# Kernel tuning notes

Measured on AMD Instinct MI355X. Metric: run time of the kernel, lower is better.

Reference implementation:

```python
import jax, jax.numpy as jnp
import numpy as np


def setup_inputs() -> dict:
    key = jax.random.key(0)
    k1, k2 = jax.random.split(key)
    B, T, F, H = 64, 512, 512, 1024
    x = jax.random.normal(k1, (B, T, F), dtype=jnp.float32)
    W = jax.random.normal(k2, (F + H, H), dtype=jnp.float32) * (1.0 / np.sqrt(F + H))
    b = jnp.zeros((H,), dtype=jnp.float32)
    return {"x": x, "W": W, "b": b}


def reference(x, W, b):
    # Vanilla tanh RNN: state_t = tanh([x_t, state_{t-1}] @ W + b); return last state.
    B, T, F = x.shape
    H = b.shape[0]
    Wx, Wh = W[:F], W[F:]  # split weight: input part [F,H], recurrent part [H,H]
    # Precompute input projections for all timesteps in one big GEMM.
    xproj = jnp.einsum('btf,fh->bth', x, Wx) + b  # [B,T,H]

    def step(state, xp_t):
        state = jnp.tanh(xp_t + state @ Wh)
        return state, None

    state0 = jnp.zeros((B, H), dtype=x.dtype)
    final_state, _ = jax.lax.scan(step, state0, jnp.swapaxes(xproj, 0, 1))
    return final_state
```

## Files before the change

kernel.cpp:

```cpp
#include <hip/hip_runtime.h>


typedef _Float16 f16;
typedef _Float16 f16x8 __attribute__((ext_vector_type(8)));
typedef _Float16 f16x4 __attribute__((ext_vector_type(4)));
typedef float f32x4 __attribute__((ext_vector_type(4)));
typedef unsigned long long u64;
typedef unsigned u32;

#define B_  64
#define T_  512
#define F_  512
#define H_  1024

#define XPH_OFF  0ull
#define WXT_OFF  67108864ull
#define WHT_OFF  68157440ull
#define SBUF_OFF 70254592ull
#define WS_NEED  70516736ull

#define ALD64(p)    __hip_atomic_load((const u64*)(p), __ATOMIC_RELAXED, __HIP_MEMORY_SCOPE_AGENT)
#define AST64(p, v) __hip_atomic_store((u64*)(p), (v), __ATOMIC_RELAXED, __HIP_MEMORY_SCOPE_AGENT)

__global__ __launch_bounds__(256) void k_init(u64* __restrict__ sbuf) {
  const unsigned i = blockIdx.x * 256 + threadIdx.x;
  sbuf[i] = (i >= 16384) ? 1ull : 0ull;
}

__global__ __launch_bounds__(256) void k_prep(const float* __restrict__ W,
                                              f16* __restrict__ WxT,
                                              f16* __restrict__ WhT) {
  __shared__ float tile[32][33];
  const int tid = threadIdx.x;
  const int kt = blockIdx.x >> 5;
  const int ht = blockIdx.x & 31;
#pragma unroll
  for (int p = 0; p < 4; ++p) {
    int kr = p * 8 + (tid >> 5);
    tile[kr][tid & 31] = W[(size_t)(kt * 32 + kr) * 1024 + ht * 32 + (tid & 31)];
  }
  __syncthreads();
  const int hl = tid >> 3;
  const int kq = tid & 7;
  f16x4 v;
#pragma unroll
  for (int j = 0; j < 4; ++j) v[j] = (f16)tile[kq * 4 + j][hl];
  const int h = ht * 32 + hl;
  const int kg = kt * 32 + kq * 4;
  if (kg < 512) *(f16x4*)(WxT + (size_t)h * 512 + kg) = v;
  else          *(f16x4*)(WhT + (size_t)h * 1024 + (kg - 512)) = v;
}

__global__ __launch_bounds__(256) void k_xproj(const float* __restrict__ x,
                                               const f16* __restrict__ WxT,
                                               const float* __restrict__ bias,
                                               f16* __restrict__ xph) {
  __shared__ __align__(16) unsigned char Al[65536];
  __shared__ __align__(16) unsigned char Bl[65536];
  const int tid = threadIdx.x;
  const int l = tid & 63, w = tid >> 6;
  const int lane15 = l & 15, sub = l >> 4;
  const int m0 = blockIdx.x * 64;
  const int bidx = m0 >> 9;
  const int t0 = m0 & 511;

  {
    const int r = tid >> 2, qq = tid & 3;
    const float* xs = x + (size_t)(m0 + r) * 512;
#pragma unroll
    for (int i = 0; i < 16; ++i) {
      int s = qq * 16 + i;
      int c = s ^ (r & 7);
      const float4 f0 = *(const float4*)(xs + c * 8);
      const float4 f1 = *(const float4*)(xs + c * 8 + 4);
      f16x8 v;
      v[0] = (f16)f0.x; v[1] = (f16)f0.y; v[2] = (f16)f0.z; v[3] = (f16)f0.w;
      v[4] = (f16)f1.x; v[5] = (f16)f1.y; v[6] = (f16)f1.z; v[7] = (f16)f1.w;
      *(f16x8*)(Al + r * 1024 + s * 16) = v;
    }
  }

  const int mh = (w >> 1) * 32, nh = (w & 1) * 32;
  const int rA0 = mh + lane15, rA1 = mh + 16 + lane15;
  const int rB0 = nh + lane15, rB1 = nh + 16 + lane15;

  for (int nb = 0; nb < 16; ++nb) {
    const int n0 = nb * 64;
    __syncthreads();
    {
      const int r = tid >> 2, qq = tid & 3;
      const f16* bs = WxT + (size_t)(n0 + r) * 512;
#pragma unroll
      for (int i = 0; i < 16; ++i) {
        int s = qq * 16 + i;
        int c = s ^ (r & 7);
        f16x8 v = *(const f16x8*)(bs + c * 8);
        *(f16x8*)(Bl + r * 1024 + s * 16) = v;
      }
    }
    __syncthreads();
    f32x4 acc00 = {0.f,0.f,0.f,0.f}, acc01 = {0.f,0.f,0.f,0.f};
    f32x4 acc10 = {0.f,0.f,0.f,0.f}, acc11 = {0.f,0.f,0.f,0.f};
#pragma unroll
    for (int kk = 0; kk < 16; ++kk) {
      const int s = kk * 4 + sub;
      f16x8 a0 = *(const f16x8*)(Al + rA0 * 1024 + ((s ^ (rA0 & 7)) << 4));
      f16x8 a1 = *(const f16x8*)(Al + rA1 * 1024 + ((s ^ (rA1 & 7)) << 4));
      f16x8 b0 = *(const f16x8*)(Bl + rB0 * 1024 + ((s ^ (rB0 & 7)) << 4));
      f16x8 b1 = *(const f16x8*)(Bl + rB1 * 1024 + ((s ^ (rB1 & 7)) << 4));
      acc00 = __builtin_amdgcn_mfma_f32_16x16x32_f16(a0, b0, acc00, 0, 0, 0);
      acc01 = __builtin_amdgcn_mfma_f32_16x16x32_f16(a0, b1, acc01, 0, 0, 0);
      acc10 = __builtin_amdgcn_mfma_f32_16x16x32_f16(a1, b0, acc10, 0, 0, 0);
      acc11 = __builtin_amdgcn_mfma_f32_16x16x32_f16(a1, b1, acc11, 0, 0, 0);
    }
    const float bv0 = bias[n0 + nh + lane15];
    const float bv1 = bias[n0 + nh + 16 + lane15];
#pragma unroll
    for (int j = 0; j < 4; ++j) {
      const int r0 = mh + sub * 4 + j;
      const int r1 = mh + 16 + sub * 4 + j;
      const size_t row0 = (size_t)(t0 + r0) * 64 + bidx;
      const size_t row1 = (size_t)(t0 + r1) * 64 + bidx;
      xph[row0 * 1024 + n0 + nh + lane15]      = (f16)(acc00[j] + bv0);
      xph[row0 * 1024 + n0 + nh + 16 + lane15] = (f16)(acc01[j] + bv1);
      xph[row1 * 1024 + n0 + nh + lane15]      = (f16)(acc10[j] + bv0);
      xph[row1 * 1024 + n0 + nh + 16 + lane15] = (f16)(acc11[j] + bv1);
    }
  }
}

__global__ __launch_bounds__(256, 1) void k_rnn(const f16* __restrict__ xph,
                                                const f16* __restrict__ WhT,
                                                f16* sbuf,
                                                float* __restrict__ out) {
  __shared__ __align__(16) unsigned char lds[131072 + 2176];
  unsigned char* WhL  = lds;
  unsigned char* stL  = lds + 98304;
  unsigned char* tbuf = lds + 131072;
  const int tid = threadIdx.x;
  const int l = tid & 63, w = tid >> 6;
  const int lane15 = l & 15, sub = l >> 4;
  const int bid = blockIdx.x;
  const int group = (bid & 7) >> 1;
  const int slice = (bid >> 3) * 2 + (bid & 1);

  for (int i = 0; i < 24; ++i) {
    int s = i * 256 + tid;
    int r = s / 96;
    int ks = 32 + (s - r * 96);
    f16x8 v = *(const f16x8*)(WhT + (size_t)(slice * 64 + r) * 1024 + ks * 8);
    *(f16x8*)(WhL + r * 1536 + ((ks ^ (r & 7)) - 32) * 16) = v;
  }
  const int colL = slice * 64 + w * 16 + lane15;
  f16x8 breg[8];
  {
    const f16* src = WhT + (size_t)colL * 1024 + sub * 8;
#pragma unroll
    for (int kk = 0; kk < 8; ++kk) breg[kk] = *(const f16x8*)(src + kk * 32);
  }
  const int rA = lane15, xA = rA & 7;
  const int rB = w * 16 + lane15, xB = rB & 7;
  const unsigned char* stLb = stL + rA * 2048;
  const unsigned char* whb  = WhL + rB * 1536;

  const int p = tid >> 4, q = tid & 15;
  const int c0s = slice * 64 + w * 16 + sub * 4;
  const int stoff = lane15 * 2048 + (((c0s >> 3) ^ (lane15 & 7)) << 4) + (c0s & 7) * 2;

  for (int t = 0; t < T_; ++t) {
    const char* ib = (const char*)sbuf + (size_t)(t & 1) * 131072 + group * 32768;
    char*       ob = (char*)sbuf + (size_t)((t + 1) & 1) * 131072 + group * 32768;

    float xpv[4];
#pragma unroll
    for (int j = 0; j < 4; ++j)
      xpv[j] = (float)xph[(size_t)(t * 64 + group * 16 + sub * 4 + j) * 1024 + colL];

    {
      u64 tmp[16];
      const char* src = ib + p * 128 + q * 8;
#pragma unroll
      for (int i = 0; i < 16; ++i) tmp[i] = ALD64(src + i * 2048);
      const u32 want = (u32)((t >> 1) & 1);
      for (;;) {
        u32 bad = 0;
#pragma unroll
        for (int i = 0; i < 16; ++i) bad |= ((u32)tmp[i] ^ want) & 1u;
        if (bad == 0) break;
#pragma unroll
        for (int i = 0; i < 16; ++i) tmp[i] = ALD64(src + i * 2048);
      }
#pragma unroll
      for (int i = 0; i < 16; ++i)
        *(u64*)(stL + i * 2048 + p * 128 + q * 8) = tmp[i];
    }
    __syncthreads();

    f32x4 acc0 = {0.f,0.f,0.f,0.f}, acc1 = {0.f,0.f,0.f,0.f};
#pragma unroll
    for (int kk = 0; kk < 32; ++kk) {
      const int s = kk * 4 + sub;
      f16x8 a = *(const f16x8*)(stLb + ((s ^ xA) << 4));
      f16x8 b = (kk < 8) ? breg[kk]
                         : *(const f16x8*)(whb + (((s ^ xB) - 32) << 4));
      if (kk & 1) acc1 = __builtin_amdgcn_mfma_f32_16x16x32_f16(a, b, acc1, 0, 0, 0);
      else        acc0 = __builtin_amdgcn_mfma_f32_16x16x32_f16(a, b, acc0, 0, 0, 0);
    }

    if (t == T_ - 1) {
#pragma unroll
      for (int j = 0; j < 4; ++j) {
        const int r = sub * 4 + j;
        out[(size_t)(group * 16 + r) * 1024 + colL] =
            tanhf(acc0[j] + acc1[j] + xpv[j]);
      }
      break;
    }

#pragma unroll
    for (int j = 0; j < 4; ++j) {
      f16 hv = (f16)tanhf(acc0[j] + acc1[j] + xpv[j]);
      *(f16*)(tbuf + (sub * 4 + j) * 136 + (w * 16 + lane15) * 2) = hv;
    }
    asm volatile("s_waitcnt lgkmcnt(0)" ::: "memory");
    {
      u64 packed = *(const u64*)(tbuf + lane15 * 136 + (w * 16 + sub * 4) * 2);
      packed = (packed & ~1ull) | (u64)(((t + 1) >> 1) & 1);
      AST64(ob + stoff, packed);
    }
    __syncthreads();
  }
}

extern "C" void kernel_launch(void* const* d_in, const int* in_sizes, int n_in,
                              void* d_out, int out_size, void* d_ws, size_t ws_size,
                              hipStream_t stream) {
  const float* x    = (const float*)d_in[0];
  const float* W    = (const float*)d_in[1];
  const float* bias = (const float*)d_in[2];
  float* out = (float*)d_out;
  char* w = (char*)d_ws;

  f16* xph = (f16*)(w + XPH_OFF);
  f16* WxT = (f16*)(w + WXT_OFF);
  f16* WhT = (f16*)(w + WHT_OFF);
  f16* sbuf = (f16*)(w + SBUF_OFF);

  k_init<<<dim3(128), dim3(256), 0, stream>>>((u64*)(w + SBUF_OFF));

  k_prep<<<dim3(48 * 32), dim3(256), 0, stream>>>(W, WxT, WhT);
  k_xproj<<<dim3(512), dim3(256), 0, stream>>>(x, WxT, bias, xph);
  k_rnn<<<dim3(64), dim3(256), 0, stream>>>(xph, WhT, sbuf, out);
}
```

Before: 1.775 ms.

## Ping-pong two batch groups per block to overlap state exchange with MFMA

Each persistent RNN block now owns two batch groups. It alternates between them, so the global state exchange and spin-wait for one group overlap with the matrix-multiply of the other. The grid is halved to 32 blocks, each covering a 64-column slice for two groups. More Wh columns are kept in registers and the LDS tile shrinks. tanhf is replaced by an exp/rcp approximation, which trades some accuracy for fewer instructions on the serial critical path.

```diff
diff --git a/kernel.cpp b/kernel.cpp
--- a/kernel.cpp
+++ b/kernel.cpp
@@ -21,6 +21,14 @@
 
 #define ALD64(p)    __hip_atomic_load((const u64*)(p), __ATOMIC_RELAXED, __HIP_MEMORY_SCOPE_AGENT)
 #define AST64(p, v) __hip_atomic_store((u64*)(p), (v), __ATOMIC_RELAXED, __HIP_MEMORY_SCOPE_AGENT)
+
+__device__ __forceinline__ float fast_tanh(float x) {
+  float e;
+  asm("v_exp_f32 %0, %1" : "=v"(e) : "v"(x * 2.885390081777927f));
+  float r;
+  asm("v_rcp_f32 %0, %1" : "=v"(r) : "v"(e + 1.0f));
+  return 1.0f - 2.0f * r;
+}
 
 __global__ __launch_bounds__(256) void k_init(u64* __restrict__ sbuf) {
   const unsigned i = blockIdx.x * 256 + threadIdx.x;
@@ -133,102 +141,170 @@
                                                 const f16* __restrict__ WhT,
                                                 f16* sbuf,
                                                 float* __restrict__ out) {
-  __shared__ __align__(16) unsigned char lds[131072 + 2176];
+  __shared__ __align__(16) unsigned char lds[149632];
   unsigned char* WhL  = lds;
-  unsigned char* stL  = lds + 98304;
-  unsigned char* tbuf = lds + 131072;
+  unsigned char* stA  = lds + 81920;
+  unsigned char* stB  = lds + 114688;
+  unsigned char* tbuf = lds + 147456;
   const int tid = threadIdx.x;
   const int l = tid & 63, w = tid >> 6;
   const int lane15 = l & 15, sub = l >> 4;
   const int bid = blockIdx.x;
-  const int group = (bid & 7) >> 1;
-  const int slice = (bid >> 3) * 2 + (bid & 1);
-
-  for (int i = 0; i < 24; ++i) {
+  const int pair = bid & 1, slice = bid >> 1;
+  const int gA = pair * 2, gB = pair * 2 + 1;
+
+  for (int i = 0; i < 20; ++i) {
     int s = i * 256 + tid;
-    int r = s / 96;
-    int ks = 32 + (s - r * 96);
+    int r = s / 80;
+    int ks = 48 + (s - r * 80);
     f16x8 v = *(const f16x8*)(WhT + (size_t)(slice * 64 + r) * 1024 + ks * 8);
-    *(f16x8*)(WhL + r * 1536 + ((ks ^ (r & 7)) - 32) * 16) = v;
+    *(f16x8*)(WhL + r * 1280 + ((ks ^ (r & 7)) - 48) * 16) = v;
   }
   const int colL = slice * 64 + w * 16 + lane15;
-  f16x8 breg[8];
+  f16x8 breg[12];
   {
     const f16* src = WhT + (size_t)colL * 1024 + sub * 8;
 #pragma unroll
-    for (int kk = 0; kk < 8; ++kk) breg[kk] = *(const f16x8*)(src + kk * 32);
-  }
+    for (int kk = 0; kk < 12; ++kk) breg[kk] = *(const f16x8*)(src + kk * 32);
+  }
+#pragma unroll
+  for (int kk = 0; kk < 12; ++kk) asm volatile("" : "+v"(breg[kk]));
+
   const int rA = lane15, xA = rA & 7;
   const int rB = w * 16 + lane15, xB = rB & 7;
-  const unsigned char* stLb = stL + rA * 2048;
-  const unsigned char* whb  = WhL + rB * 1536;
+  const unsigned char* whb = WhL + rB * 1280;
+  const unsigned char* stAb = stA + rA * 2048;
+  const unsigned char* stBb = stB + rA * 2048;
 
   const int p = tid >> 4, q = tid & 15;
   const int c0s = slice * 64 + w * 16 + sub * 4;
   const int stoff = lane15 * 2048 + (((c0s >> 3) ^ (lane15 & 7)) << 4) + (c0s & 7) * 2;
+  const size_t baseA = (size_t)gA * 32768, baseB = (size_t)gB * 32768;
+
+#pragma unroll
+  for (int i = 0; i < 16; ++i) *(u64*)(stA + i * 2048 + tid * 8) = 0ull;
+  float xpvA[4], xpvB[4];
+#pragma unroll
+  for (int j = 0; j < 4; ++j)
+    xpvA[j] = (float)xph[(size_t)(gA * 16 + sub * 4 + j) * 1024 + colL];
+  __syncthreads();
 
   for (int t = 0; t < T_; ++t) {
-    const char* ib = (const char*)sbuf + (size_t)(t & 1) * 131072 + group * 32768;
-    char*       ob = (char*)sbuf + (size_t)((t + 1) & 1) * 131072 + group * 32768;
-
-    float xpv[4];
-#pragma unroll
-    for (int j = 0; j < 4; ++j)
-      xpv[j] = (float)xph[(size_t)(t * 64 + group * 16 + sub * 4 + j) * 1024 + colL];
-
     {
       u64 tmp[16];
-      const char* src = ib + p * 128 + q * 8;
+      const char* src = (const char*)sbuf + (size_t)(t & 1) * 131072 + baseB + p * 128 + q * 8;
 #pragma unroll
       for (int i = 0; i < 16; ++i) tmp[i] = ALD64(src + i * 2048);
-      const u32 want = (u32)((t >> 1) & 1);
-      for (;;) {
-        u32 bad = 0;
-#pragma unroll
-        for (int i = 0; i < 16; ++i) bad |= ((u32)tmp[i] ^ want) & 1u;
-        if (bad == 0) break;
+#pragma unroll
+      for (int j = 0; j < 4; ++j)
+        xpvB[j] = (float)xph[(size_t)(t * 64 + gB * 16 + sub * 4 + j) * 1024 + colL];
+
+      f32x4 acc0 = {0.f,0.f,0.f,0.f}, acc1 = {0.f,0.f,0.f,0.f};
+#pragma unroll
+      for (int kk = 0; kk < 32; ++kk) {
+        const int s = kk * 4 + sub;
+        f16x8 a = *(const f16x8*)(stAb + ((s ^ xA) << 4));
+        f16x8 b = (kk < 12) ? breg[kk]
+                            : *(const f16x8*)(whb + (((s ^ xB) - 48) << 4));
+        if (kk & 1) acc1 = __builtin_amdgcn_mfma_f32_16x16x32_f16(a, b, acc1, 0, 0, 0);
+        else        acc0 = __builtin_amdgcn_mfma_f32_16x16x32_f16(a, b, acc0, 0, 0, 0);
+      }
+      float rv[4];
+#pragma unroll
+      for (int j = 0; j < 4; ++j) rv[j] = acc0[j] + acc1[j] + xpvA[j];
+
+      if (t == T_ - 1) {
+#pragma unroll
+        for (int j = 0; j < 4; ++j)
+          out[(size_t)(gA * 16 + sub * 4 + j) * 1024 + colL] = fast_tanh(rv[j]);
+      } else {
+#pragma unroll
+        for (int j = 0; j < 4; ++j) {
+          f16 hv = (f16)fast_tanh(rv[j]);
+          *(f16*)(tbuf + (sub * 4 + j) * 136 + (w * 16 + lane15) * 2) = hv;
+        }
+        asm volatile("s_waitcnt lgkmcnt(0)" ::: "memory");
+        u64 packed = *(const u64*)(tbuf + lane15 * 136 + (w * 16 + sub * 4) * 2);
+        packed = (packed & ~1ull) | (u64)(((t + 1) >> 1) & 1);
+        char* dst = (char*)sbuf + (size_t)((t + 1) & 1) * 131072 + baseA + stoff;
+        AST64(dst, packed);
+      }
+
+      {
+        const u32 want = (u32)((t >> 1) & 1);
+        for (;;) {
+          u32 bad = 0;
+#pragma unroll
+          for (int i = 0; i < 16; ++i) bad |= ((u32)tmp[i] ^ want) & 1u;
+          if (bad == 0) break;
+#pragma unroll
+          for (int i = 0; i < 16; ++i) tmp[i] = ALD64(src + i * 2048);
+        }
+#pragma unroll
+        for (int i = 0; i < 16; ++i)
+          *(u64*)(stB + i * 2048 + p * 128 + q * 8) = tmp[i];
+      }
+      __syncthreads();
+    }
+
+    {
+      u64 tmp[16];
+      const char* src = (const char*)sbuf + (size_t)((t + 1) & 1) * 131072 + baseA + p * 128 + q * 8;
+      if (t < T_ - 1) {
 #pragma unroll
         for (int i = 0; i < 16; ++i) tmp[i] = ALD64(src + i * 2048);
-      }
-#pragma unroll
-      for (int i = 0; i < 16; ++i)
-        *(u64*)(stL + i * 2048 + p * 128 + q * 8) = tmp[i];
-    }
-    __syncthreads();
-
-    f32x4 acc0 = {0.f,0.f,0.f,0.f}, acc1 = {0.f,0.f,0.f,0.f};
-#pragma unroll
-    for (int kk = 0; kk < 32; ++kk) {
-      const int s = kk * 4 + sub;
-      f16x8 a = *(const f16x8*)(stLb + ((s ^ xA) << 4));
-      f16x8 b = (kk < 8) ? breg[kk]
-                         : *(const f16x8*)(whb + (((s ^ xB) - 32) << 4));
-      if (kk & 1) acc1 = __builtin_amdgcn_mfma_f32_16x16x32_f16(a, b, acc1, 0, 0, 0);
-      else        acc0 = __builtin_amdgcn_mfma_f32_16x16x32_f16(a, b, acc0, 0, 0, 0);
-    }
-
-    if (t == T_ - 1) {
+#pragma unroll
+        for (int j = 0; j < 4; ++j)
+          xpvA[j] = (float)xph[(size_t)((t + 1) * 64 + gA * 16 + sub * 4 + j) * 1024 + colL];
+      }
+
+      f32x4 acc0 = {0.f,0.f,0.f,0.f}, acc1 = {0.f,0.f,0.f,0.f};
+#pragma unroll
+      for (int kk = 0; kk < 32; ++kk) {
+        const int s = kk * 4 + sub;
+        f16x8 a = *(const f16x8*)(stBb + ((s ^ xA) << 4));
+        f16x8 b = (kk < 12) ? breg[kk]
+                            : *(const f16x8*)(whb + (((s ^ xB) - 48) << 4));
+        if (kk & 1) acc1 = __builtin_amdgcn_mfma_f32_16x16x32_f16(a, b, acc1, 0, 0, 0);
+        else        acc0 = __builtin_amdgcn_mfma_f32_16x16x32_f16(a, b, acc0, 0, 0, 0);
+      }
+      float rv[4];
+#pragma unroll
+      for (int j = 0; j < 4; ++j) rv[j] = acc0[j] + acc1[j] + xpvB[j];
+
+      if (t == T_ - 1) {
+#pragma unroll
+        for (int j = 0; j < 4; ++j)
+          out[(size_t)(gB * 16 + sub * 4 + j) * 1024 + colL] = fast_tanh(rv[j]);
+        break;
+      }
 #pragma unroll
       for (int j = 0; j < 4; ++j) {
-        const int r = sub * 4 + j;
-        out[(size_t)(group * 16 + r) * 1024 + colL] =
-            tanhf(acc0[j] + acc1[j] + xpv[j]);
-      }
-      break;
-    }
-
-#pragma unroll
-    for (int j = 0; j < 4; ++j) {
-      f16 hv = (f16)tanhf(acc0[j] + acc1[j] + xpv[j]);
-      *(f16*)(tbuf + (sub * 4 + j) * 136 + (w * 16 + lane15) * 2) = hv;
-    }
-    asm volatile("s_waitcnt lgkmcnt(0)" ::: "memory");
-    {
+        f16 hv = (f16)fast_tanh(rv[j]);
+        *(f16*)(tbuf + (sub * 4 + j) * 136 + (w * 16 + lane15) * 2) = hv;
+      }
+      asm volatile("s_waitcnt lgkmcnt(0)" ::: "memory");
       u64 packed = *(const u64*)(tbuf + lane15 * 136 + (w * 16 + sub * 4) * 2);
       packed = (packed & ~1ull) | (u64)(((t + 1) >> 1) & 1);
-      AST64(ob + stoff, packed);
-    }
-    __syncthreads();
+      char* dst = (char*)sbuf + (size_t)((t + 1) & 1) * 131072 + baseB + stoff;
+      AST64(dst, packed);
+
+      {
+        const u32 want = (u32)(((t + 1) >> 1) & 1);
+        for (;;) {
+          u32 bad = 0;
+#pragma unroll
+          for (int i = 0; i < 16; ++i) bad |= ((u32)tmp[i] ^ want) & 1u;
+          if (bad == 0) break;
+#pragma unroll
+          for (int i = 0; i < 16; ++i) tmp[i] = ALD64(src + i * 2048);
+        }
+#pragma unroll
+        for (int i = 0; i < 16; ++i)
+          *(u64*)(stA + i * 2048 + p * 128 + q * 8) = tmp[i];
+      }
+      __syncthreads();
+    }
   }
 }
 
@@ -250,5 +326,5 @@
 
   k_prep<<<dim3(48 * 32), dim3(256), 0, stream>>>(W, WxT, WhT);
   k_xproj<<<dim3(512), dim3(256), 0, stream>>>(x, WxT, bias, xph);
-  k_rnn<<<dim3(64), dim3(256), 0, stream>>>(xph, WhT, sbuf, out);
-}
+  k_rnn<<<dim3(32), dim3(256), 0, stream>>>(xph, WhT, sbuf, out);
+}
```

Result: slower. 2.678 ms (+50.9%).

## Read recurrent state fragments directly from global, drop LDS staging and barriers

Applied to the files above, without the earlier changes.

Each wave now loads its MFMA A-operand fragments of the previous state straight from the global exchange buffer and polls per k-chunk on the parity flag bits. This replaces the bulk copy into LDS and both per-step __syncthreads, so MFMAs can start as soon as early chunks arrive. The state layout drops the XOR swizzle, the block-to-group mapping changes, MFMA accumulators are split four ways, and tanhf is replaced with an exp/rcp approximation. In exchange, each wave issues more redundant global loads, and the fast tanh loses some accuracy near zero.

```diff
diff --git a/kernel.cpp b/kernel.cpp
--- a/kernel.cpp
+++ b/kernel.cpp
@@ -7,6 +7,7 @@
 typedef float f32x4 __attribute__((ext_vector_type(4)));
 typedef unsigned long long u64;
 typedef unsigned u32;
+typedef unsigned long long u64x2 __attribute__((ext_vector_type(2)));
 
 #define B_  64
 #define T_  512
@@ -21,6 +22,14 @@
 
 #define ALD64(p)    __hip_atomic_load((const u64*)(p), __ATOMIC_RELAXED, __HIP_MEMORY_SCOPE_AGENT)
 #define AST64(p, v) __hip_atomic_store((u64*)(p), (v), __ATOMIC_RELAXED, __HIP_MEMORY_SCOPE_AGENT)
+
+__device__ __forceinline__ float fast_tanh(float x) {
+  float e;
+  asm("v_exp_f32 %0, %1" : "=v"(e) : "v"(x * 2.885390081777927f));
+  float r;
+  asm("v_rcp_f32 %0, %1" : "=v"(r) : "v"(e + 1.0f));
+  return 1.0f - 2.0f * r;
+}
 
 __global__ __launch_bounds__(256) void k_init(u64* __restrict__ sbuf) {
   const unsigned i = blockIdx.x * 256 + threadIdx.x;
@@ -133,16 +142,15 @@
                                                 const f16* __restrict__ WhT,
                                                 f16* sbuf,
                                                 float* __restrict__ out) {
-  __shared__ __align__(16) unsigned char lds[131072 + 2176];
+  __shared__ __align__(16) unsigned char lds[98304 + 2176];
   unsigned char* WhL  = lds;
-  unsigned char* stL  = lds + 98304;
-  unsigned char* tbuf = lds + 131072;
+  unsigned char* tbuf = lds + 98304;
   const int tid = threadIdx.x;
   const int l = tid & 63, w = tid >> 6;
   const int lane15 = l & 15, sub = l >> 4;
   const int bid = blockIdx.x;
-  const int group = (bid & 7) >> 1;
-  const int slice = (bid >> 3) * 2 + (bid & 1);
+  const int group = bid & 3;
+  const int slice = bid >> 2;
 
   for (int i = 0; i < 24; ++i) {
     int s = i * 256 + tid;
@@ -158,68 +166,73 @@
 #pragma unroll
     for (int kk = 0; kk < 8; ++kk) breg[kk] = *(const f16x8*)(src + kk * 32);
   }
-  const int rA = lane15, xA = rA & 7;
+#pragma unroll
+  for (int kk = 0; kk < 8; ++kk) asm volatile("" : "+v"(breg[kk]));
+  __syncthreads();
+
   const int rB = w * 16 + lane15, xB = rB & 7;
-  const unsigned char* stLb = stL + rA * 2048;
-  const unsigned char* whb  = WhL + rB * 1536;
-
-  const int p = tid >> 4, q = tid & 15;
-  const int c0s = slice * 64 + w * 16 + sub * 4;
-  const int stoff = lane15 * 2048 + (((c0s >> 3) ^ (lane15 & 7)) << 4) + (c0s & 7) * 2;
+  const unsigned char* whb = WhL + rB * 1536;
+
+  const int fragoff = lane15 * 2048 + sub * 16;
+  const int c0 = slice * 64 + w * 16 + sub * 4;
+  const int stoff = lane15 * 2048 + c0 * 2;
+  const size_t gbase = (size_t)group * 32768;
 
   for (int t = 0; t < T_; ++t) {
-    const char* ib = (const char*)sbuf + (size_t)(t & 1) * 131072 + group * 32768;
-    char*       ob = (char*)sbuf + (size_t)((t + 1) & 1) * 131072 + group * 32768;
+    const char* ib = (const char*)sbuf + (size_t)(t & 1) * 131072 + gbase;
+    char*       ob = (char*)sbuf + (size_t)((t + 1) & 1) * 131072 + gbase;
 
     float xpv[4];
 #pragma unroll
     for (int j = 0; j < 4; ++j)
       xpv[j] = (float)xph[(size_t)(t * 64 + group * 16 + sub * 4 + j) * 1024 + colL];
 
-    {
-      u64 tmp[16];
-      const char* src = ib + p * 128 + q * 8;
-#pragma unroll
-      for (int i = 0; i < 16; ++i) tmp[i] = ALD64(src + i * 2048);
-      const u32 want = (u32)((t >> 1) & 1);
-      for (;;) {
-        u32 bad = 0;
-#pragma unroll
-        for (int i = 0; i < 16; ++i) bad |= ((u32)tmp[i] ^ want) & 1u;
-        if (bad == 0) break;
-#pragma unroll
-        for (int i = 0; i < 16; ++i) tmp[i] = ALD64(src + i * 2048);
+    const char* rb = ib + fragoff;
+    const u32 want = (u32)((t >> 1) & 1);
+
+    u64 lo[8], hi[8];
+#pragma unroll
+    for (int i = 0; i < 8; ++i) {
+      lo[i] = ALD64(rb + i * 64);
+      hi[i] = ALD64(rb + i * 64 + 8);
+    }
+    f32x4 acc[4];
+#pragma unroll
+    for (int i = 0; i < 4; ++i) acc[i] = (f32x4){0.f, 0.f, 0.f, 0.f};
+
+#pragma unroll
+    for (int kk = 0; kk < 32; ++kk) {
+      u64 L = lo[kk & 7], H = hi[kk & 7];
+      while (__any((int)((((u32)L ^ want) | ((u32)H ^ want)) & 1u))) {
+        L = ALD64(rb + kk * 64);
+        H = ALD64(rb + kk * 64 + 8);
       }
-#pragma unroll
-      for (int i = 0; i < 16; ++i)
-        *(u64*)(stL + i * 2048 + p * 128 + q * 8) = tmp[i];
-    }
-    __syncthreads();
-
-    f32x4 acc0 = {0.f,0.f,0.f,0.f}, acc1 = {0.f,0.f,0.f,0.f};
-#pragma unroll
-    for (int kk = 0; kk < 32; ++kk) {
+      if (kk < 24) {
+        lo[kk & 7] = ALD64(rb + (kk + 8) * 64);
+        hi[kk & 7] = ALD64(rb + (kk + 8) * 64 + 8);
+      }
+      u64x2 pk; pk[0] = L; pk[1] = H;
+      f16x8 a = __builtin_bit_cast(f16x8, pk);
       const int s = kk * 4 + sub;
-      f16x8 a = *(const f16x8*)(stLb + ((s ^ xA) << 4));
       f16x8 b = (kk < 8) ? breg[kk]
                          : *(const f16x8*)(whb + (((s ^ xB) - 32) << 4));
-      if (kk & 1) acc1 = __builtin_amdgcn_mfma_f32_16x16x32_f16(a, b, acc1, 0, 0, 0);
-      else        acc0 = __builtin_amdgcn_mfma_f32_16x16x32_f16(a, b, acc0, 0, 0, 0);
-    }
+      acc[kk & 3] = __builtin_amdgcn_mfma_f32_16x16x32_f16(a, b, acc[kk & 3], 0, 0, 0);
+    }
+    float rv[4];
+#pragma unroll
+    for (int j = 0; j < 4; ++j)
+      rv[j] = acc[0][j] + acc[1][j] + acc[2][j] + acc[3][j] + xpv[j];
 
     if (t == T_ - 1) {
 #pragma unroll
-      for (int j = 0; j < 4; ++j) {
-        const int r = sub * 4 + j;
-        out[(size_t)(group * 16 + r) * 1024 + colL] =
-            tanhf(acc0[j] + acc1[j] + xpv[j]);
-      }
+      for (int j = 0; j < 4; ++j)
+        out[(size_t)(group * 16 + sub * 4 + j) * 1024 + colL] = fast_tanh(rv[j]);
       break;
     }
 
 #pragma unroll
     for (int j = 0; j < 4; ++j) {
-      f16 hv = (f16)tanhf(acc0[j] + acc1[j] + xpv[j]);
+      f16 hv = (f16)fast_tanh(rv[j]);
       *(f16*)(tbuf + (sub * 4 + j) * 136 + (w * 16 + lane15) * 2) = hv;
     }
     asm volatile("s_waitcnt lgkmcnt(0)" ::: "memory");
@@ -228,7 +241,6 @@
       packed = (packed & ~1ull) | (u64)(((t + 1) >> 1) & 1);
       AST64(ob + stoff, packed);
     }
-    __syncthreads();
   }
 }
 
```

After: 5.933 ms. 3.34x slower.

## Double-buffer RNN state in LDS, drop trailing barrier, use fast tanh

Applied to the files above, without the earlier changes.

Gives the recurrent state two LDS buffers that alternate by timestep, which lets the end-of-step __syncthreads be removed so each step has only one barrier. It also moves more Wh columns into registers (10 k-chunks instead of 8), shrinking the LDS-resident slice, and spreads the MFMAs over four accumulators to shorten dependency chains. The spin-wait now keeps two polling loads in flight, and tanhf is replaced by an exp/rcp approximation. The approximation costs accuracy, and the extra registers could hurt scheduling.

```diff
diff --git a/kernel.cpp b/kernel.cpp
--- a/kernel.cpp
+++ b/kernel.cpp
@@ -21,6 +21,14 @@
 
 #define ALD64(p)    __hip_atomic_load((const u64*)(p), __ATOMIC_RELAXED, __HIP_MEMORY_SCOPE_AGENT)
 #define AST64(p, v) __hip_atomic_store((u64*)(p), (v), __ATOMIC_RELAXED, __HIP_MEMORY_SCOPE_AGENT)
+
+__device__ __forceinline__ float fast_tanh(float x) {
+  float e;
+  asm("v_exp_f32 %0, %1" : "=v"(e) : "v"(x * 2.885390081777927f));
+  float r;
+  asm("v_rcp_f32 %0, %1" : "=v"(r) : "v"(e + 1.0f));
+  return 1.0f - 2.0f * r;
+}
 
 __global__ __launch_bounds__(256) void k_init(u64* __restrict__ sbuf) {
   const unsigned i = blockIdx.x * 256 + threadIdx.x;
@@ -133,10 +141,11 @@
                                                 const f16* __restrict__ WhT,
                                                 f16* sbuf,
                                                 float* __restrict__ out) {
-  __shared__ __align__(16) unsigned char lds[131072 + 2176];
+  __shared__ __align__(16) unsigned char lds[157824];
   unsigned char* WhL  = lds;
-  unsigned char* stL  = lds + 98304;
-  unsigned char* tbuf = lds + 131072;
+  unsigned char* stL0 = lds + 90112;
+  unsigned char* stL1 = lds + 122880;
+  unsigned char* tbuf = lds + 155648;
   const int tid = threadIdx.x;
   const int l = tid & 63, w = tid >> 6;
   const int lane15 = l & 15, sub = l >> 4;
@@ -144,32 +153,36 @@
   const int group = (bid & 7) >> 1;
   const int slice = (bid >> 3) * 2 + (bid & 1);
 
-  for (int i = 0; i < 24; ++i) {
+  for (int i = 0; i < 22; ++i) {
     int s = i * 256 + tid;
-    int r = s / 96;
-    int ks = 32 + (s - r * 96);
+    int r = s / 88;
+    int ks = 40 + (s - r * 88);
     f16x8 v = *(const f16x8*)(WhT + (size_t)(slice * 64 + r) * 1024 + ks * 8);
-    *(f16x8*)(WhL + r * 1536 + ((ks ^ (r & 7)) - 32) * 16) = v;
+    *(f16x8*)(WhL + r * 1408 + ((ks ^ (r & 7)) - 40) * 16) = v;
   }
   const int colL = slice * 64 + w * 16 + lane15;
-  f16x8 breg[8];
+  f16x8 breg[10];
   {
     const f16* src = WhT + (size_t)colL * 1024 + sub * 8;
 #pragma unroll
-    for (int kk = 0; kk < 8; ++kk) breg[kk] = *(const f16x8*)(src + kk * 32);
-  }
+    for (int kk = 0; kk < 10; ++kk) breg[kk] = *(const f16x8*)(src + kk * 32);
+  }
+#pragma unroll
+  for (int kk = 0; kk < 10; ++kk) asm volatile("" : "+v"(breg[kk]));
+
   const int rA = lane15, xA = rA & 7;
   const int rB = w * 16 + lane15, xB = rB & 7;
-  const unsigned char* stLb = stL + rA * 2048;
-  const unsigned char* whb  = WhL + rB * 1536;
+  const unsigned char* whb = WhL + rB * 1408;
 
   const int p = tid >> 4, q = tid & 15;
+  const int cmt = p * 128 + q * 8;
   const int c0s = slice * 64 + w * 16 + sub * 4;
   const int stoff = lane15 * 2048 + (((c0s >> 3) ^ (lane15 & 7)) << 4) + (c0s & 7) * 2;
 
   for (int t = 0; t < T_; ++t) {
     const char* ib = (const char*)sbuf + (size_t)(t & 1) * 131072 + group * 32768;
     char*       ob = (char*)sbuf + (size_t)((t + 1) & 1) * 131072 + group * 32768;
+    unsigned char* stC = (t & 1) ? stL1 : stL0;
 
     float xpv[4];
 #pragma unroll
@@ -177,49 +190,65 @@
       xpv[j] = (float)xph[(size_t)(t * 64 + group * 16 + sub * 4 + j) * 1024 + colL];
 
     {
-      u64 tmp[16];
-      const char* src = ib + p * 128 + q * 8;
-#pragma unroll
-      for (int i = 0; i < 16; ++i) tmp[i] = ALD64(src + i * 2048);
+      const char* src = ib + cmt;
       const u32 want = (u32)((t >> 1) & 1);
+      u64 tA[16], tB[16];
+#pragma unroll
+      for (int i = 0; i < 16; ++i) tA[i] = ALD64(src + i * 2048);
+#pragma unroll
+      for (int i = 0; i < 16; ++i) tB[i] = ALD64(src + i * 2048);
       for (;;) {
         u32 bad = 0;
 #pragma unroll
-        for (int i = 0; i < 16; ++i) bad |= ((u32)tmp[i] ^ want) & 1u;
-        if (bad == 0) break;
-#pragma unroll
-        for (int i = 0; i < 16; ++i) tmp[i] = ALD64(src + i * 2048);
+        for (int i = 0; i < 16; ++i) bad |= ((u32)tA[i] ^ want) & 1u;
+        if (!bad) {
+#pragma unroll
+          for (int i = 0; i < 16; ++i) *(u64*)(stC + i * 2048 + cmt) = tA[i];
+          break;
+        }
+#pragma unroll
+        for (int i = 0; i < 16; ++i) tA[i] = ALD64(src + i * 2048);
+        bad = 0;
+#pragma unroll
+        for (int i = 0; i < 16; ++i) bad |= ((u32)tB[i] ^ want) & 1u;
+        if (!bad) {
+#pragma unroll
+          for (int i = 0; i < 16; ++i) *(u64*)(stC + i * 2048 + cmt) = tB[i];
+          break;
+        }
+#pragma unroll
+        for (int i = 0; i < 16; ++i) tB[i] = ALD64(src + i * 2048);
       }
-#pragma unroll
-      for (int i = 0; i < 16; ++i)
-        *(u64*)(stL + i * 2048 + p * 128 + q * 8) = tmp[i];
     }
     __syncthreads();
 
-    f32x4 acc0 = {0.f,0.f,0.f,0.f}, acc1 = {0.f,0.f,0.f,0.f};
+    const unsigned char* stLb = stC + rA * 2048;
+    f32x4 acc[4];
+#pragma unroll
+    for (int i = 0; i < 4; ++i) acc[i] = (f32x4){0.f, 0.f, 0.f, 0.f};
 #pragma unroll
     for (int kk = 0; kk < 32; ++kk) {
       const int s = kk * 4 + sub;
       f16x8 a = *(const f16x8*)(stLb + ((s ^ xA) << 4));
-      f16x8 b = (kk < 8) ? breg[kk]
-                         : *(const f16x8*)(whb + (((s ^ xB) - 32) << 4));
-      if (kk & 1) acc1 = __builtin_amdgcn_mfma_f32_16x16x32_f16(a, b, acc1, 0, 0, 0);
-      else        acc0 = __builtin_amdgcn_mfma_f32_16x16x32_f16(a, b, acc0, 0, 0, 0);
-    }
+      f16x8 b = (kk < 10) ? breg[kk]
+                          : *(const f16x8*)(whb + (((s ^ xB) - 40) << 4));
+      acc[kk & 3] = __builtin_amdgcn_mfma_f32_16x16x32_f16(a, b, acc[kk & 3], 0, 0, 0);
+    }
+    float rv[4];
+#pragma unroll
+    for (int j = 0; j < 4; ++j)
+      rv[j] = acc[0][j] + acc[1][j] + acc[2][j] + acc[3][j] + xpv[j];
 
     if (t == T_ - 1) {
 #pragma unroll
-      for (int j = 0; j < 4; ++j) {
-        const int r = sub * 4 + j;
-        out[(size_t)(group * 16 + r) * 1024 + colL] =
-            tanhf(acc0[j] + acc1[j] + xpv[j]);
-      }
+      for (int j = 0; j < 4; ++j)
+        out[(size_t)(group * 16 + sub * 4 + j) * 1024 + colL] = fast_tanh(rv[j]);
       break;
     }
 
 #pragma unroll
     for (int j = 0; j < 4; ++j) {
-      f16 hv = (f16)tanhf(acc0[j] + acc1[j] + xpv[j]);
+      f16 hv = (f16)fast_tanh(rv[j]);
       *(f16*)(tbuf + (sub * 4 + j) * 136 + (w * 16 + lane15) * 2) = hv;
     }
     asm volatile("s_waitcnt lgkmcnt(0)" ::: "memory");
@@ -228,7 +257,6 @@
       packed = (packed & ~1ull) | (u64)(((t + 1) >> 1) & 1);
       AST64(ob + stoff, packed);
     }
-    __syncthreads();
   }
 }
 
```

Result: slower. 1.867 ms (+5.2%).
